# Optimization experiments

Measured on AMD Instinct MI355X. Metric: run time of the kernel, lower is better.

## Reference

```python
import jax, jax.numpy as jnp
import numpy as np

N, K, D, H = 100000, 16, 128, 4
HD = D // H
EPS = 1e-5


def layer_norm(x, g, b):
    mu = jnp.mean(x, axis=-1, keepdims=True)
    var = jnp.mean(jnp.square(x - mu), axis=-1, keepdims=True)
    return (x - mu) * jax.lax.rsqrt(var + EPS) * g + b


def setup_inputs() -> dict:
    key = jax.random.key(0)
    ks = jax.random.split(key, 8)
    s = 0.02
    x = jax.random.normal(ks[0], (N, D), jnp.float32)
    attention_samples = jax.random.randint(ks[1], (N, K), 0, N)
    in_proj_w = jax.random.normal(ks[2], (3 * D, D), jnp.float32) * s
    in_proj_b = jnp.zeros((3 * D,), jnp.float32)
    out_w = jax.random.normal(ks[3], (D, D), jnp.float32) * s
    out_b = jnp.zeros((D,), jnp.float32)
    ffn_w1 = jax.random.normal(ks[4], (4 * D, D), jnp.float32) * s
    ffn_b1 = jnp.zeros((4 * D,), jnp.float32)
    ffn_w2 = jax.random.normal(ks[5], (D, 4 * D), jnp.float32) * s
    ffn_b2 = jnp.zeros((D,), jnp.float32)
    ln1_g = jnp.ones((D,), jnp.float32)
    ln1_b = jnp.zeros((D,), jnp.float32)
    ln2_g = jnp.ones((D,), jnp.float32)
    ln2_b = jnp.zeros((D,), jnp.float32)
    return dict(x=x, attention_samples=attention_samples, in_proj_w=in_proj_w,
                in_proj_b=in_proj_b, out_w=out_w, out_b=out_b,
                ffn_w1=ffn_w1, ffn_b1=ffn_b1, ffn_w2=ffn_w2, ffn_b2=ffn_b2,
                ln1_g=ln1_g, ln1_b=ln1_b, ln2_g=ln2_g, ln2_b=ln2_b)


def reference(x, attention_samples, in_proj_w, in_proj_b, out_w, out_b,
              ffn_w1, ffn_b1, ffn_w2, ffn_b2, ln1_g, ln1_b, ln2_g, ln2_b):
    n = x.shape[0]
    k = attention_samples.shape[1]
    wq, wk, wv = in_proj_w[:D], in_proj_w[D:2 * D], in_proj_w[2 * D:]
    bq, bk, bv = in_proj_b[:D], in_proj_b[D:2 * D], in_proj_b[2 * D:]
    # Project first (one [N,D] GEMM each), then gather the projections.
    # Mathematically identical to torch's gather-then-project (projection is per-row linear).
    q = x @ wq.T + bq                      # [N, D]
    kx = x @ wk.T + bk                     # [N, D]
    vx = x @ wv.T + bv                     # [N, D]
    k_s = kx[attention_samples]            # [N, K, D]
    v_s = vx[attention_samples]            # [N, K, D]
    qh = q.reshape(n, H, HD)               # [N, H, HD]
    kh = k_s.reshape(n, k, H, HD)          # [N, K, H, HD]
    vh = v_s.reshape(n, k, H, HD)
    scores = jnp.einsum('nhd,nkhd->nhk', qh, kh) / np.sqrt(HD).astype(np.float32)
    w = jax.nn.softmax(scores, axis=-1)    # [N, H, K]
    attn = jnp.einsum('nhk,nkhd->nhd', w, vh).reshape(n, D)
    attn = attn @ out_w.T + out_b          # out_proj
    x = layer_norm(x + attn, ln1_g, ln1_b)
    h = jax.nn.relu(x @ ffn_w1.T + ffn_b1)
    x = layer_norm(x + h @ ffn_w2.T + ffn_b2, ln2_g, ln2_b)
    return x
```

## Files before the change

### kernel.cpp

```cpp
#include <hip/hip_runtime.h>
#include <hip/hip_bf16.h>
#include <hip/hip_fp8.h>

#define NTOK 100000
#define EPS 1e-5f

using frag  = __attribute__((ext_vector_type(8))) short;
using f32x4 = __attribute__((ext_vector_type(4))) float;
typedef __hip_bfloat16 bf16;
typedef unsigned short ushort_t;

__device__ inline float bits2f(unsigned int u) { union { unsigned int i; float f; } x; x.i = u; return x.f; }
__device__ inline void bfu_unpack(unsigned int u, float& lo, float& hi) {
  lo = bits2f(u << 16);
  hi = bits2f(u & 0xffff0000u);
}

__device__ inline float4 fp8x4_to_f4(unsigned int u) {
  __hip_fp8_e4m3 a, b, c, d;
  a.__x = u & 0xff; b.__x = (u >> 8) & 0xff; c.__x = (u >> 16) & 0xff; d.__x = (u >> 24) & 0xff;
  return make_float4((float)a, (float)b, (float)c, (float)d);
}
__device__ inline unsigned char f_to_fp8(float f) { __hip_fp8_e4m3 t(f); return t.__x; }

__global__ __launch_bounds__(256) void cvt_x_kernel(const float* __restrict__ in,
                                                    bf16* __restrict__ out) {
  const int e = (blockIdx.x * 256 + threadIdx.x) * 4;
  float4 v = *(const float4*)&in[e];
  bf16 o[4] = {__float2bfloat16(v.x), __float2bfloat16(v.y),
               __float2bfloat16(v.z), __float2bfloat16(v.w)};
  *(ulong1*)&out[e] = *(ulong1*)o;
}

__global__ __launch_bounds__(256) void cvt_w_kernel(
    const float* __restrict__ w0, const float* __restrict__ w1,
    const float* __restrict__ w2, const float* __restrict__ w3,
    bf16* __restrict__ out) {
  const int e = (blockIdx.x * 256 + threadIdx.x) * 4;
  const float* src;
  int off;
  if (e < 49152)       { src = w0; off = 0; }
  else if (e < 65536)  { src = w1; off = 49152; }
  else if (e < 131072) { src = w2; off = 65536; }
  else                 { src = w3; off = 131072; }
  float4 v = *(const float4*)&src[e - off];
  bf16 o[4] = {__float2bfloat16(v.x), __float2bfloat16(v.y),
               __float2bfloat16(v.z), __float2bfloat16(v.w)};
  *(ulong1*)&out[e] = *(ulong1*)o;
}

template<int KSTEPS>
__device__ __forceinline__ void gemm_body(
    const bf16* __restrict__ A,
    const bf16* __restrict__ Wslab,
    int row0, int M, ushort_t* Bs, f32x4 (&acc)[2][8]) {
  const int KTOT = KSTEPS * 128;
  const int tid = threadIdx.x;
  const int lane = tid & 63;
  const int lr = lane & 15, kg = lane >> 4;

  int r0 = row0 + lr;      if (r0 > M - 1) r0 = M - 1;
  int r1 = row0 + 16 + lr; if (r1 > M - 1) r1 = M - 1;
  const bf16* a0 = A + (size_t)r0 * KTOT + kg * 8;
  const bf16* a1 = A + (size_t)r1 * KTOT + kg * 8;

  frag a[2][4];
#pragma unroll
  for (int kc = 0; kc < 4; ++kc) {
    a[0][kc] = *(const frag*)(a0 + kc * 32);
    a[1][kc] = *(const frag*)(a1 + kc * 32);
  }

  uint4 sreg[8];
#pragma unroll
  for (int r = 0; r < 8; ++r) {
    const int g = r * 256 + tid, row = g >> 4, u = g & 15;
    sreg[r] = *(const uint4*)(Wslab + (size_t)row * KTOT + (u ^ (row & 15)) * 8);
  }
#pragma unroll
  for (int r = 0; r < 8; ++r) {
    const int g = r * 256 + tid, row = g >> 4, u = g & 15;
    *(uint4*)&Bs[row * 128 + u * 8] = sreg[r];
  }
  __syncthreads();

#pragma unroll
  for (int c = 0; c < KSTEPS; ++c) {
    if (c > 0) {
#pragma unroll
      for (int kc = 0; kc < 4; ++kc) {
        a[0][kc] = *(const frag*)(a0 + c * 128 + kc * 32);
        a[1][kc] = *(const frag*)(a1 + c * 128 + kc * 32);
      }
    }
    if (c + 1 < KSTEPS) {
#pragma unroll
      for (int r = 0; r < 8; ++r) {
        const int g = r * 256 + tid, row = g >> 4, u = g & 15;
        sreg[r] = *(const uint4*)(Wslab + (size_t)row * KTOT + (c + 1) * 128 +
                                  (u ^ (row & 15)) * 8);
      }
    }
#pragma unroll
    for (int kc = 0; kc < 4; ++kc) {
#pragma unroll
      for (int j = 0; j < 8; ++j) {
        frag b = *(const frag*)&Bs[(lr + 16 * j) * 128 + (((kc * 4 + kg) ^ lr) * 8)];
        acc[0][j] = __builtin_amdgcn_mfma_f32_16x16x32_bf16(a[0][kc], b, acc[0][j], 0, 0, 0);
        acc[1][j] = __builtin_amdgcn_mfma_f32_16x16x32_bf16(a[1][kc], b, acc[1][j], 0, 0, 0);
      }
    }
    if (c + 1 < KSTEPS) {
      __syncthreads();
#pragma unroll
      for (int r = 0; r < 8; ++r) {
        const int g = r * 256 + tid, row = g >> 4, u = g & 15;
        *(uint4*)&Bs[row * 128 + u * 8] = sreg[r];
      }
      __syncthreads();
    }
  }
}

__global__ __launch_bounds__(256, 4) void k_qkv(
    const bf16* __restrict__ A, const bf16* __restrict__ W,
    const float* __restrict__ bias, bf16* __restrict__ qout,
    unsigned char* __restrict__ kout, unsigned char* __restrict__ vout, int M) {
  __shared__ ushort_t Bs[16384];
  const int lane = threadIdx.x & 63;
  const int wid = threadIdx.x >> 6;
  const int row0 = blockIdx.x * 128 + wid * 32;
  const int cbase = blockIdx.y * 128;
  const int lr = lane & 15, kg = lane >> 4;

  f32x4 acc[2][8] = {};
  gemm_body<1>(A, W + (size_t)cbase * 128, row0, M, Bs, acc);

  float bs[8];
#pragma unroll
  for (int j = 0; j < 8; ++j) bs[j] = bias[cbase + lr + 16 * j];
  const int y = blockIdx.y;
  unsigned char* f8dst = (y == 1) ? kout : vout;
#pragma unroll
  for (int i = 0; i < 2; ++i)
#pragma unroll
    for (int r = 0; r < 4; ++r) {
      const int row = row0 + 16 * i + 4 * kg + r;
      if (row >= M) continue;
      if (y == 0) {
        bf16* orow = qout + (size_t)row * 128 + lr;
#pragma unroll
        for (int j = 0; j < 8; ++j) orow[16 * j] = __float2bfloat16(acc[i][j][r] + bs[j]);
      } else {
        unsigned char* orow = f8dst + (size_t)row * 128 + lr;
#pragma unroll
        for (int j = 0; j < 8; ++j) orow[16 * j] = f_to_fp8(acc[i][j][r] + bs[j]);
      }
    }
}

__global__ __launch_bounds__(256, 4) void k_ffn1(
    const bf16* __restrict__ A, const bf16* __restrict__ W,
    const float* __restrict__ bias, bf16* __restrict__ out, int M) {
  __shared__ ushort_t Bs[16384];
  const int lane = threadIdx.x & 63;
  const int wid = threadIdx.x >> 6;
  const int row0 = blockIdx.x * 128 + wid * 32;
  const int cbase = blockIdx.y * 128;
  const int lr = lane & 15, kg = lane >> 4;

  f32x4 acc[2][8] = {};
  gemm_body<1>(A, W + (size_t)cbase * 128, row0, M, Bs, acc);

  float bs[8];
#pragma unroll
  for (int j = 0; j < 8; ++j) bs[j] = bias[cbase + lr + 16 * j];
#pragma unroll
  for (int i = 0; i < 2; ++i)
#pragma unroll
    for (int r = 0; r < 4; ++r) {
      const int row = row0 + 16 * i + 4 * kg + r;
      if (row >= M) continue;
      bf16* orow = out + (size_t)row * 512 + cbase + lr;
#pragma unroll
      for (int j = 0; j < 8; ++j)
        orow[16 * j] = __float2bfloat16(fmaxf(acc[i][j][r] + bs[j], 0.f));
    }
}

__global__ __launch_bounds__(256, 4) void k_outproj_ln(
    const bf16* __restrict__ A, const bf16* __restrict__ W,
    const float* __restrict__ bias, const bf16* __restrict__ resid,
    const float* __restrict__ g, const float* __restrict__ b,
    bf16* __restrict__ out, int M) {
  __shared__ ushort_t Bs[16384];
  const int lane = threadIdx.x & 63;
  const int wid = threadIdx.x >> 6;
  const int row0 = blockIdx.x * 128 + wid * 32;
  const int lr = lane & 15, kg = lane >> 4;

  f32x4 acc[2][8] = {};
  gemm_body<1>(A, W, row0, M, Bs, acc);

  float bs[8], gs[8], bbs[8];
#pragma unroll
  for (int j = 0; j < 8; ++j) {
    const int c = lr + 16 * j;
    bs[j] = bias[c]; gs[j] = g[c]; bbs[j] = b[c];
  }
#pragma unroll
  for (int i = 0; i < 2; ++i)
#pragma unroll
    for (int r = 0; r < 4; ++r) {
      const int row = row0 + 16 * i + 4 * kg + r;
      const int rr = (row > M - 1) ? (M - 1) : row;
      const bf16* rrow = resid + (size_t)rr * 128 + lr;
      float v[8], psum = 0.f, psq = 0.f;
#pragma unroll
      for (int j = 0; j < 8; ++j) {
        v[j] = acc[i][j][r] + bs[j] + __bfloat162float(rrow[16 * j]);
        psum += v[j];
        psq += v[j] * v[j];
      }
#pragma unroll
      for (int off = 1; off < 16; off <<= 1) {
        psum += __shfl_xor(psum, off);
        psq += __shfl_xor(psq, off);
      }
      const float mean = psum * (1.f / 128.f);
      const float var = psq * (1.f / 128.f) - mean * mean;
      const float rstd = rsqrtf(var + EPS);
      if (row < M) {
        bf16* orow = out + (size_t)row * 128 + lr;
#pragma unroll
        for (int j = 0; j < 8; ++j)
          orow[16 * j] = __float2bfloat16((v[j] - mean) * rstd * gs[j] + bbs[j]);
      }
    }
}

__global__ __launch_bounds__(256, 3) void k_ffn2_ln(
    const bf16* __restrict__ A,
    const bf16* __restrict__ W,
    const float* __restrict__ bias, const bf16* __restrict__ resid,
    const float* __restrict__ g, const float* __restrict__ b,
    float* __restrict__ out, int M) {
  __shared__ ushort_t Bs[16384];
  const int lane = threadIdx.x & 63;
  const int wid = threadIdx.x >> 6;
  const int row0 = blockIdx.x * 128 + wid * 32;
  const int lr = lane & 15, kg = lane >> 4;

  f32x4 acc[2][8] = {};
  gemm_body<4>(A, W, row0, M, Bs, acc);

  float bs[8], gs[8], bbs[8];
#pragma unroll
  for (int j = 0; j < 8; ++j) {
    const int c = lr + 16 * j;
    bs[j] = bias[c]; gs[j] = g[c]; bbs[j] = b[c];
  }
#pragma unroll
  for (int i = 0; i < 2; ++i)
#pragma unroll
    for (int r = 0; r < 4; ++r) {
      const int row = row0 + 16 * i + 4 * kg + r;
      const int rr = (row > M - 1) ? (M - 1) : row;
      const bf16* rrow = resid + (size_t)rr * 128 + lr;
      float v[8], psum = 0.f, psq = 0.f;
#pragma unroll
      for (int j = 0; j < 8; ++j) {
        v[j] = acc[i][j][r] + bs[j] + __bfloat162float(rrow[16 * j]);
        psum += v[j];
        psq += v[j] * v[j];
      }
#pragma unroll
      for (int off = 1; off < 16; off <<= 1) {
        psum += __shfl_xor(psum, off);
        psq += __shfl_xor(psq, off);
      }
      const float mean = psum * (1.f / 128.f);
      const float var = psq * (1.f / 128.f) - mean * mean;
      const float rstd = rsqrtf(var + EPS);
      if (row < M) {
        float* orow = out + (size_t)row * 128 + lr;
#pragma unroll
        for (int j = 0; j < 8; ++j)
          orow[16 * j] = (v[j] - mean) * rstd * gs[j] + bbs[j];
      }
    }
}

__global__ __launch_bounds__(256) void attn_kernel(
    const bf16* __restrict__ qb, const unsigned char* __restrict__ kf8,
    const unsigned char* __restrict__ vf8, const int* __restrict__ samples,
    bf16* __restrict__ attn) {
  const int lane = threadIdx.x & 63;
  const int wid = threadIdx.x >> 6;
  const int tok = blockIdx.x * 4 + wid;
  if (tok >= NTOK) return;
  const int qt = lane >> 4;
  const int lr = lane & 15;

  const float scale = 0.17677669529663687f;
  float q8[8];
  {
    uint4 qu = *(const uint4*)&qb[(size_t)tok * 128 + 8 * lr];
    bfu_unpack(qu.x, q8[0], q8[1]);
    bfu_unpack(qu.y, q8[2], q8[3]);
    bfu_unpack(qu.z, q8[4], q8[5]);
    bfu_unpack(qu.w, q8[6], q8[7]);
#pragma unroll
    for (int d = 0; d < 8; ++d) q8[d] *= scale;
  }

  const int myidx = samples[tok * 16 + lr];
  int kidx[4];
#pragma unroll
  for (int jj = 0; jj < 4; ++jj) kidx[jj] = __shfl(myidx, 4 * jj + qt, 16);

  float s[4];
#pragma unroll
  for (int jj = 0; jj < 4; ++jj) {
    uint2 ku = *(const uint2*)&kf8[(size_t)kidx[jj] * 128 + 8 * lr];
    float4 k0 = fp8x4_to_f4(ku.x), k1 = fp8x4_to_f4(ku.y);
    float p = q8[0] * k0.x + q8[1] * k0.y + q8[2] * k0.z + q8[3] * k0.w +
              q8[4] * k1.x + q8[5] * k1.y + q8[6] * k1.z + q8[7] * k1.w;
    p += __shfl_xor(p, 1);
    p += __shfl_xor(p, 2);
    s[jj] = p;
  }

  float m = fmaxf(fmaxf(s[0], s[1]), fmaxf(s[2], s[3]));
  m = fmaxf(m, __shfl_xor(m, 16));
  m = fmaxf(m, __shfl_xor(m, 32));
  float sum = 0.f;
#pragma unroll
  for (int jj = 0; jj < 4; ++jj) {
    s[jj] = __expf(s[jj] - m);
    sum += s[jj];
  }
  sum += __shfl_xor(sum, 16);
  sum += __shfl_xor(sum, 32);
  const float inv = 1.f / sum;

  float a8[8] = {};
#pragma unroll
  for (int jj = 0; jj < 4; ++jj) {
    uint2 vu = *(const uint2*)&vf8[(size_t)kidx[jj] * 128 + 8 * lr];
    float4 v0 = fp8x4_to_f4(vu.x), v1 = fp8x4_to_f4(vu.y);
    const float wj = s[jj] * inv;
    a8[0] += wj * v0.x; a8[1] += wj * v0.y; a8[2] += wj * v0.z; a8[3] += wj * v0.w;
    a8[4] += wj * v1.x; a8[5] += wj * v1.y; a8[6] += wj * v1.z; a8[7] += wj * v1.w;
  }
#pragma unroll
  for (int d = 0; d < 8; ++d) {
    a8[d] += __shfl_xor(a8[d], 16);
    a8[d] += __shfl_xor(a8[d], 32);
  }

  if (qt == 0) {
    uint4 o;
    o.x = (unsigned)__bfloat16_as_ushort(__float2bfloat16(a8[0])) |
          ((unsigned)__bfloat16_as_ushort(__float2bfloat16(a8[1])) << 16);
    o.y = (unsigned)__bfloat16_as_ushort(__float2bfloat16(a8[2])) |
          ((unsigned)__bfloat16_as_ushort(__float2bfloat16(a8[3])) << 16);
    o.z = (unsigned)__bfloat16_as_ushort(__float2bfloat16(a8[4])) |
          ((unsigned)__bfloat16_as_ushort(__float2bfloat16(a8[5])) << 16);
    o.w = (unsigned)__bfloat16_as_ushort(__float2bfloat16(a8[6])) |
          ((unsigned)__bfloat16_as_ushort(__float2bfloat16(a8[7])) << 16);
    *(uint4*)&attn[(size_t)tok * 128 + 8 * lr] = o;
  }
}

extern "C" void kernel_launch(void* const* d_in, const int* in_sizes, int n_in,
                              void* d_out, int out_size, void* d_ws, size_t ws_size,
                              hipStream_t stream) {
  const float* x      = (const float*)d_in[0];
  const int* samples  = (const int*)d_in[1];
  const float* in_w   = (const float*)d_in[2];
  const float* in_b   = (const float*)d_in[3];
  const float* out_w  = (const float*)d_in[4];
  const float* out_b  = (const float*)d_in[5];
  const float* ffn_w1 = (const float*)d_in[6];
  const float* ffn_b1 = (const float*)d_in[7];
  const float* ffn_w2 = (const float*)d_in[8];
  const float* ffn_b2 = (const float*)d_in[9];
  const float* ln1_g  = (const float*)d_in[10];
  const float* ln1_b  = (const float*)d_in[11];
  const float* ln2_g  = (const float*)d_in[12];
  const float* ln2_b  = (const float*)d_in[13];
  float* out = (float*)d_out;

  char* ws = (char*)d_ws;
  bf16* xb   = (bf16*)(ws);
  bf16* qb   = (bf16*)(ws + 25600000);
  unsigned char* kf8 = (unsigned char*)(ws + 51200000);
  unsigned char* vf8 = (unsigned char*)(ws + 64000000);
  bf16* attn = (bf16*)(ws + 76800000);
  bf16* h    = (bf16*)(ws);
  bf16* x1b  = (bf16*)(ws + 102400000);
  bf16* wb   = (bf16*)(ws + 128000000);
  bf16* in_wb   = wb;
  bf16* out_wb  = wb + 49152;
  bf16* ffn_w1b = wb + 65536;
  bf16* ffn_w2b = wb + 131072;

  const int M = NTOK;
  dim3 blk(256);
  const int gm = (M + 127) / 128;

  cvt_x_kernel<<<dim3(12500), blk, 0, stream>>>(x, xb);
  cvt_w_kernel<<<dim3(192), blk, 0, stream>>>(in_w, out_w, ffn_w1, ffn_w2, wb);
  k_qkv<<<dim3(gm, 3), blk, 0, stream>>>(xb, in_wb, in_b, qb, kf8, vf8, M);
  attn_kernel<<<dim3((M + 3) / 4), blk, 0, stream>>>(qb, kf8, vf8, samples, attn);
  k_outproj_ln<<<dim3(gm), blk, 0, stream>>>(attn, out_wb, out_b, xb, ln1_g, ln1_b, x1b, M);
  k_ffn1<<<dim3(gm, 4), blk, 0, stream>>>(x1b, ffn_w1b, ffn_b1, h, M);
  k_ffn2_ln<<<dim3(gm), blk, 0, stream>>>(h, ffn_w2b, ffn_b2, x1b, ln2_g, ln2_b, out, M);
}
```

Baseline: 229.5 us.

## Stage A tiles through swizzled LDS with coalesced loads in GEMM body

The shared GEMM body now loads the A (activation) tile cooperatively into a second XOR-swizzled LDS buffer using coalesced 16-byte loads. Previously each wave read its A fragments straight from global memory in a strided per-lane pattern. Both A and B next-step tiles are prefetched into registers during the MFMA loop. This doubles LDS use per block to 64 KB and raises register pressure, so launch bounds are lowered to 2 blocks per CU, which reduces occupancy.

```diff
diff --git a/kernel.cpp b/kernel.cpp
--- a/kernel.cpp
+++ b/kernel.cpp
@@ -52,80 +52,78 @@
 template<int KSTEPS>
 __device__ __forceinline__ void gemm_body(
     const bf16* __restrict__ A,
-    const bf16* __restrict__ Wslab,
-    int row0, int M, ushort_t* Bs, f32x4 (&acc)[2][8]) {
+    const bf16* __restrict__ W,
+    int row0, int M, ushort_t* As, ushort_t* Bs, f32x4 (&acc)[2][8]) {
   const int KTOT = KSTEPS * 128;
   const int tid = threadIdx.x;
   const int lane = tid & 63;
+  const int wid = tid >> 6;
   const int lr = lane & 15, kg = lane >> 4;
-
-  int r0 = row0 + lr;      if (r0 > M - 1) r0 = M - 1;
-  int r1 = row0 + 16 + lr; if (r1 > M - 1) r1 = M - 1;
-  const bf16* a0 = A + (size_t)r0 * KTOT + kg * 8;
-  const bf16* a1 = A + (size_t)r1 * KTOT + kg * 8;
-
-  frag a[2][4];
-#pragma unroll
-  for (int kc = 0; kc < 4; ++kc) {
-    a[0][kc] = *(const frag*)(a0 + kc * 32);
-    a[1][kc] = *(const frag*)(a1 + kc * 32);
-  }
-
-  uint4 sreg[8];
+  const int rb = tid >> 4;
+  const int uu = tid & 15;
+  const int su = uu ^ rb;
+
+  const bf16* agp[8];
+  const bf16* bgp[8];
 #pragma unroll
   for (int r = 0; r < 8; ++r) {
-    const int g = r * 256 + tid, row = g >> 4, u = g & 15;
-    sreg[r] = *(const uint4*)(Wslab + (size_t)row * KTOT + (u ^ (row & 15)) * 8);
-  }
-#pragma unroll
-  for (int r = 0; r < 8; ++r) {
-    const int g = r * 256 + tid, row = g >> 4, u = g & 15;
-    *(uint4*)&Bs[row * 128 + u * 8] = sreg[r];
-  }
+    int grow = row0 + r * 16 + rb;
+    if (grow > M - 1) grow = M - 1;
+    agp[r] = A + (size_t)grow * KTOT + su * 8;
+    bgp[r] = W + (size_t)(r * 16 + rb) * KTOT + su * 8;
+  }
+  const int lslot = rb * 128 + uu * 8;
+
+  uint4 sa[8], sb[8];
+#define SLOAD(c)                                                  \
+  {                                                               \
+    _Pragma("unroll") for (int r = 0; r < 8; ++r) {               \
+      sa[r] = *(const uint4*)(agp[r] + (c) * 128);                \
+      sb[r] = *(const uint4*)(bgp[r] + (c) * 128);                \
+    }                                                             \
+  }
+#define SWRITE()                                                  \
+  {                                                               \
+    _Pragma("unroll") for (int r = 0; r < 8; ++r) {               \
+      *(uint4*)&As[lslot + r * 2048] = sa[r];                     \
+      *(uint4*)&Bs[lslot + r * 2048] = sb[r];                     \
+    }                                                             \
+  }
+
+  SLOAD(0);
+  SWRITE();
   __syncthreads();
 
 #pragma unroll
   for (int c = 0; c < KSTEPS; ++c) {
-    if (c > 0) {
-#pragma unroll
-      for (int kc = 0; kc < 4; ++kc) {
-        a[0][kc] = *(const frag*)(a0 + c * 128 + kc * 32);
-        a[1][kc] = *(const frag*)(a1 + c * 128 + kc * 32);
-      }
-    }
-    if (c + 1 < KSTEPS) {
-#pragma unroll
-      for (int r = 0; r < 8; ++r) {
-        const int g = r * 256 + tid, row = g >> 4, u = g & 15;
-        sreg[r] = *(const uint4*)(Wslab + (size_t)row * KTOT + (c + 1) * 128 +
-                                  (u ^ (row & 15)) * 8);
-      }
-    }
+    if (c + 1 < KSTEPS) SLOAD(c + 1);
 #pragma unroll
     for (int kc = 0; kc < 4; ++kc) {
+      const int uoff = ((kc * 4 + kg) ^ lr) * 8;
+      frag a0 = *(const frag*)&As[(wid * 32 + lr) * 128 + uoff];
+      frag a1 = *(const frag*)&As[(wid * 32 + 16 + lr) * 128 + uoff];
 #pragma unroll
       for (int j = 0; j < 8; ++j) {
-        frag b = *(const frag*)&Bs[(lr + 16 * j) * 128 + (((kc * 4 + kg) ^ lr) * 8)];
-        acc[0][j] = __builtin_amdgcn_mfma_f32_16x16x32_bf16(a[0][kc], b, acc[0][j], 0, 0, 0);
-        acc[1][j] = __builtin_amdgcn_mfma_f32_16x16x32_bf16(a[1][kc], b, acc[1][j], 0, 0, 0);
+        frag b = *(const frag*)&Bs[(lr + 16 * j) * 128 + uoff];
+        acc[0][j] = __builtin_amdgcn_mfma_f32_16x16x32_bf16(a0, b, acc[0][j], 0, 0, 0);
+        acc[1][j] = __builtin_amdgcn_mfma_f32_16x16x32_bf16(a1, b, acc[1][j], 0, 0, 0);
       }
     }
     if (c + 1 < KSTEPS) {
       __syncthreads();
-#pragma unroll
-      for (int r = 0; r < 8; ++r) {
-        const int g = r * 256 + tid, row = g >> 4, u = g & 15;
-        *(uint4*)&Bs[row * 128 + u * 8] = sreg[r];
-      }
+      SWRITE();
       __syncthreads();
     }
   }
-}
-
-__global__ __launch_bounds__(256, 4) void k_qkv(
+#undef SLOAD
+#undef SWRITE
+}
+
+__global__ __launch_bounds__(256, 2) void k_qkv(
     const bf16* __restrict__ A, const bf16* __restrict__ W,
     const float* __restrict__ bias, bf16* __restrict__ qout,
     unsigned char* __restrict__ kout, unsigned char* __restrict__ vout, int M) {
+  __shared__ ushort_t As[16384];
   __shared__ ushort_t Bs[16384];
   const int lane = threadIdx.x & 63;
   const int wid = threadIdx.x >> 6;
@@ -134,7 +132,7 @@
   const int lr = lane & 15, kg = lane >> 4;
 
   f32x4 acc[2][8] = {};
-  gemm_body<1>(A, W + (size_t)cbase * 128, row0, M, Bs, acc);
+  gemm_body<1>(A, W + (size_t)cbase * 128, blockIdx.x * 128, M, As, Bs, acc);
 
   float bs[8];
 #pragma unroll
@@ -159,9 +157,10 @@
     }
 }
 
-__global__ __launch_bounds__(256, 4) void k_ffn1(
+__global__ __launch_bounds__(256, 2) void k_ffn1(
     const bf16* __restrict__ A, const bf16* __restrict__ W,
     const float* __restrict__ bias, bf16* __restrict__ out, int M) {
+  __shared__ ushort_t As[16384];
   __shared__ ushort_t Bs[16384];
   const int lane = threadIdx.x & 63;
   const int wid = threadIdx.x >> 6;
@@ -170,7 +169,7 @@
   const int lr = lane & 15, kg = lane >> 4;
 
   f32x4 acc[2][8] = {};
-  gemm_body<1>(A, W + (size_t)cbase * 128, row0, M, Bs, acc);
+  gemm_body<1>(A, W + (size_t)cbase * 128, blockIdx.x * 128, M, As, Bs, acc);
 
   float bs[8];
 #pragma unroll
@@ -188,11 +187,12 @@
     }
 }
 
-__global__ __launch_bounds__(256, 4) void k_outproj_ln(
+__global__ __launch_bounds__(256, 2) void k_outproj_ln(
     const bf16* __restrict__ A, const bf16* __restrict__ W,
     const float* __restrict__ bias, const bf16* __restrict__ resid,
     const float* __restrict__ g, const float* __restrict__ b,
     bf16* __restrict__ out, int M) {
+  __shared__ ushort_t As[16384];
   __shared__ ushort_t Bs[16384];
   const int lane = threadIdx.x & 63;
   const int wid = threadIdx.x >> 6;
@@ -200,7 +200,7 @@
   const int lr = lane & 15, kg = lane >> 4;
 
   f32x4 acc[2][8] = {};
-  gemm_body<1>(A, W, row0, M, Bs, acc);
+  gemm_body<1>(A, W, blockIdx.x * 128, M, As, Bs, acc);
 
   float bs[8], gs[8], bbs[8];
 #pragma unroll
@@ -239,12 +239,13 @@
     }
 }
 
-__global__ __launch_bounds__(256, 3) void k_ffn2_ln(
+__global__ __launch_bounds__(256, 2) void k_ffn2_ln(
     const bf16* __restrict__ A,
     const bf16* __restrict__ W,
     const float* __restrict__ bias, const bf16* __restrict__ resid,
     const float* __restrict__ g, const float* __restrict__ b,
     float* __restrict__ out, int M) {
+  __shared__ ushort_t As[16384];
   __shared__ ushort_t Bs[16384];
   const int lane = threadIdx.x & 63;
   const int wid = threadIdx.x >> 6;
@@ -252,7 +253,7 @@
   const int lr = lane & 15, kg = lane >> 4;
 
   f32x4 acc[2][8] = {};
-  gemm_body<4>(A, W, row0, M, Bs, acc);
+  gemm_body<4>(A, W, blockIdx.x * 128, M, As, Bs, acc);
 
   float bs[8], gs[8], bbs[8];
 #pragma unroll
```

New measurement: 257.4 us. 1.12x slower.
